# Kernel optimization log

Hardware: AMD Instinct MI355X
Metric: run time of the kernel (lower is better)

## Reference

```python
import jax, jax.numpy as jnp
import numpy as np
from jax import lax

H, W = 4096, 4096

def setup_inputs() -> dict:
    key = jax.random.key(0)
    k_occ, k_seed = jax.random.split(key)
    occupied = (jax.random.uniform(k_occ, (H, W)) < 0.3).astype(jnp.float32)
    flood = ((jax.random.uniform(k_seed, (H, W)) < 1e-3).astype(jnp.float32)
             * (1.0 - occupied))
    flood_input = jnp.stack([occupied, flood], axis=-1)  # [H, W, 2]
    flood_count = jnp.zeros((H, W), dtype=jnp.float32)
    # Fixed flood kernel, HWIO layout: (3, 3, in=2, out=1)
    kernel = jnp.zeros((3, 3, 2, 1), dtype=jnp.float32)
    kernel = kernel.at[1, 1, 0, 0].set(-5.0)  # occupied center blocks flood
    kernel = kernel.at[1, 2, 1, 0].set(1.0)   # right
    kernel = kernel.at[2, 1, 1, 0].set(1.0)   # down
    kernel = kernel.at[1, 0, 1, 0].set(1.0)   # left
    kernel = kernel.at[0, 1, 1, 0].set(1.0)   # up
    kernel = kernel.at[1, 1, 1, 0].set(1.0)   # center
    bias = jnp.zeros((1,), dtype=jnp.float32)
    return {"flood_input": flood_input, "flood_count": flood_count,
            "kernel": kernel, "bias": bias, "num_steps": 16}

def reference(flood_input, flood_count, kernel, bias, num_steps):
    dn = ("NHWC", "HWIO", "NHWC")

    def flood_step(carry, _):
        x, count = carry                      # x: [H, W, 2], count: [H, W]
        occupied = x[..., 0]
        y = lax.conv_general_dilated(x[None], kernel, (1, 1), "SAME",
                                     dimension_numbers=dn)[0, ..., 0] + bias[0]
        y = jnp.clip(y, 0.0, 1.0)             # flooded frontier
        new_x = jnp.stack([occupied, y], axis=-1)
        return (new_x, count + y), None

    (x_final, count_final), _ = lax.scan(flood_step,
                                         (flood_input, flood_count),
                                         None, length=num_steps)
    # [H, W, 3]: occupied, flood, count
    return jnp.concatenate([x_final, count_final[..., None]], axis=-1)
```

## Files before the change

### kernel.cpp

```cpp
#include <hip/hip_runtime.h>


typedef unsigned long long u64;
typedef float f32x4 __attribute__((ext_vector_type(4)));
typedef float f32x2 __attribute__((ext_vector_type(2)));

#define HH 4096
#define WW 4096
#define WPR 64
#define NSTEPS 16
#define HALO 16
#define IT 32

__global__ __launch_bounds__(256) void pack_kernel(
    const float* __restrict__ flood_input,
    u64* __restrict__ occP, u64* __restrict__ flP)
{
    const int lane = threadIdx.x & 63;
    const int wv   = threadIdx.x >> 6;
    const int r    = blockIdx.x;
#pragma unroll
    for (int b = 0; b < 2; ++b) {
        float vx[8], vy[8];
#pragma unroll
        for (int j = 0; j < 8; ++j) {
            const int w = wv * 16 + b * 8 + j;
            const f32x2 v = __builtin_nontemporal_load(
                (const f32x2*)(flood_input +
                                ((size_t)r * WW + (w << 6) + lane) * 2));
            vx[j] = v[0]; vy[j] = v[1];
        }
#pragma unroll
        for (int j = 0; j < 8; ++j) {
            const int w = wv * 16 + b * 8 + j;
            const u64 om = __ballot(vx[j] > 0.5f);
            const u64 fm = __ballot(vy[j] > 0.5f);
            if (lane == 0) {
                occP[(size_t)r * WPR + w] = om;
                flP [(size_t)r * WPR + w] = fm;
            }
        }
    }
}

__global__ __launch_bounds__(256, 8) void flood_kernel(
    const u64* __restrict__ occP, const u64* __restrict__ flP,
    const float* __restrict__ flood_count,
    float* __restrict__ out)
{
    __shared__ u64 plane[4][IT][7];
    __shared__ float out2[4][2 * 128 * 3];

    const int tid  = threadIdx.x;
    const int lane = tid & 63;
    const int wv   = tid >> 6;

    const int wgid = blockIdx.y * 32 + blockIdx.x;
    const int nl   = (wgid & 7) * 512 + (wgid >> 3);
    const int bx   = nl & 31;
    const int by   = nl >> 5;

    const int tile_r0 = by * IT;
    const int tile_c0 = bx * (4 * IT) + wv * IT;
    const int bc0     = bx * (4 * IT);

    const int gr  = tile_r0 - HALO + lane;
    const bool rin = (gr >= 0) & (gr < HH);
    const int s   = tile_c0 - HALO;
    const int q0  = ((s + 64) >> 6) - 1;
    const int sh  = s - (q0 << 6);

    const size_t base = (size_t)(rin ? gr : 0) * WPR;
    const int qa = min(max(q0, 0), WPR - 1);
    const int qb = min(max(q0 + 1, 0), WPR - 1);
    u64 o0 = occP[base + qa], o1 = occP[base + qb];
    u64 f0 = flP [base + qa], f1 = flP [base + qb];
    const bool va = rin & (q0 >= 0);
    const bool vb = rin & (q0 + 1 < WPR);
    if (!va) { o0 = ~0ull; f0 = 0ull; }
    if (!vb) { o1 = ~0ull; f1 = 0ull; }
    const u64 occ = (o0 >> sh) | (sh ? (o1 << (64 - sh)) : 0ull);
    u64       f   = (f0 >> sh) | (sh ? (f1 << (64 - sh)) : 0ull);

    const int half = lane >> 5;
    const int l32  = lane & 31;
    const int col0 = l32 * 4;
    const float* fcbase = flood_count +
        (size_t)(tile_r0 + wv * 8 + half) * WW + bc0 + col0;
    f32x4 fc_next = __builtin_nontemporal_load((const f32x4*)fcbase);

    const u64 nocc = ~occ;
    u64 c0 = 0, c1 = 0, c2 = 0, c3 = 0, c4 = 0;
#pragma unroll
    for (int it = 0; it < NSTEPS; ++it) {
        u64 up = __shfl_up(f, 1);
        u64 dn = __shfl_down(f, 1);
        if (lane == 0)  up = 0ull;
        if (lane == 63) dn = 0ull;
        f = nocc & (f | (f << 1) | (f >> 1) | up | dn);
        u64 c = f, t;
        t = c0; c0 = t ^ c; c = t & c;
        t = c1; c1 = t ^ c; c = t & c;
        t = c2; c2 = t ^ c; c = t & c;
        t = c3; c3 = t ^ c; c = t & c;
        c4 ^= c;
    }

    if (lane >= HALO && lane < HALO + IT) {
        u64* p = plane[wv][lane - HALO];
        p[0] = occ; p[1] = f;
        p[2] = c0; p[3] = c1; p[4] = c2; p[5] = c3; p[6] = c4;
    }
    __syncthreads();

    const int sw   = col0 >> 5;
    const int bit0 = HALO + (col0 & 31);
    for (int t = 0; t < 4; ++t) {
        const f32x4 fc4 = fc_next;
        if (t + 1 < 4)
            fc_next = __builtin_nontemporal_load(
                (const f32x4*)(fcbase + (size_t)(t + 1) * 2 * WW));

        const int rA   = wv * 8 + 2 * t;
        const int irow = rA + half;
        const u64* p = plane[sw][irow];
        const u64 ow = p[0], fw = p[1];
        const u64 k0 = p[2], k1 = p[3], k2 = p[4], k3 = p[5], k4 = p[6];

        float v[12];
#pragma unroll
        for (int j = 0; j < 4; ++j) {
            const int bit = bit0 + j;
            int cv = (int)((k0 >> bit) & 1ull)
                   + ((int)((k1 >> bit) & 1ull) << 1)
                   + ((int)((k2 >> bit) & 1ull) << 2)
                   + ((int)((k3 >> bit) & 1ull) << 3)
                   + ((int)((k4 >> bit) & 1ull) << 4);
            v[j*3+0] = (float)((ow >> bit) & 1ull);
            v[j*3+1] = (float)((fw >> bit) & 1ull);
            v[j*3+2] = (float)cv + fc4[j];
        }
        float* dst = &out2[wv][half * 384 + l32 * 12];
        *(f32x4*)(dst + 0) = (f32x4){v[0], v[1], v[2],  v[3]};
        *(f32x4*)(dst + 4) = (f32x4){v[4], v[5], v[6],  v[7]};
        *(f32x4*)(dst + 8) = (f32x4){v[8], v[9], v[10], v[11]};

        __syncthreads();

#pragma unroll
        for (int st = 0; st < 3; ++st) {
            const int L   = st * 256 + lane * 4;
            const int row = (L >= 384) ? 1 : 0;
            const int off = L - row * 384;
            const f32x4 q = *(const f32x4*)(&out2[wv][L]);
            *(f32x4*)(out + ((size_t)(tile_r0 + rA + row) * WW + bc0) * 3
                      + off) = q;
        }
    }
}

extern "C" void kernel_launch(void* const* d_in, const int* in_sizes, int n_in,
                              void* d_out, int out_size, void* d_ws, size_t ws_size,
                              hipStream_t stream) {
    const float* flood_input = (const float*)d_in[0];
    const float* flood_cnt   = (const float*)d_in[1];
    float* out = (float*)d_out;

    u64* occP = (u64*)d_ws;
    u64* flP  = occP + (size_t)HH * WPR;

    pack_kernel<<<dim3(HH), dim3(256), 0, stream>>>(flood_input, occP, flP);

    dim3 grid(WW / (4 * IT), HH / IT);
    flood_kernel<<<grid, dim3(256), 0, stream>>>(occP, flP, flood_cnt, out);
}
```

Before: 358.7 us.

## Fuse bit-packing of the input grid into the flood kernel

Removes the separate pack kernel and its bitmask buffers in the workspace. Each wave now loads its own 64x64 halo window of float2 input straight from global memory and builds the occupancy and flood bitmasks in registers with wave ballots. This drops one kernel launch and the write-then-read of the intermediate bitmasks. In exchange, overlapping halo windows are re-read about four times per input element, and a serial 16-iteration load-and-ballot loop now sits in front of the compute.

```diff
diff --git a/kernel.cpp b/kernel.cpp
--- a/kernel.cpp
+++ b/kernel.cpp
@@ -7,44 +7,12 @@
 
 #define HH 4096
 #define WW 4096
-#define WPR 64
 #define NSTEPS 16
 #define HALO 16
 #define IT 32
 
-__global__ __launch_bounds__(256) void pack_kernel(
+__global__ __launch_bounds__(256, 8) void flood_kernel(
     const float* __restrict__ flood_input,
-    u64* __restrict__ occP, u64* __restrict__ flP)
-{
-    const int lane = threadIdx.x & 63;
-    const int wv   = threadIdx.x >> 6;
-    const int r    = blockIdx.x;
-#pragma unroll
-    for (int b = 0; b < 2; ++b) {
-        float vx[8], vy[8];
-#pragma unroll
-        for (int j = 0; j < 8; ++j) {
-            const int w = wv * 16 + b * 8 + j;
-            const f32x2 v = __builtin_nontemporal_load(
-                (const f32x2*)(flood_input +
-                                ((size_t)r * WW + (w << 6) + lane) * 2));
-            vx[j] = v[0]; vy[j] = v[1];
-        }
-#pragma unroll
-        for (int j = 0; j < 8; ++j) {
-            const int w = wv * 16 + b * 8 + j;
-            const u64 om = __ballot(vx[j] > 0.5f);
-            const u64 fm = __ballot(vy[j] > 0.5f);
-            if (lane == 0) {
-                occP[(size_t)r * WPR + w] = om;
-                flP [(size_t)r * WPR + w] = fm;
-            }
-        }
-    }
-}
-
-__global__ __launch_bounds__(256, 8) void flood_kernel(
-    const u64* __restrict__ occP, const u64* __restrict__ flP,
     const float* __restrict__ flood_count,
     float* __restrict__ out)
 {
@@ -64,30 +32,43 @@
     const int tile_c0 = bx * (4 * IT) + wv * IT;
     const int bc0     = bx * (4 * IT);
 
-    const int gr  = tile_r0 - HALO + lane;
-    const bool rin = (gr >= 0) & (gr < HH);
-    const int s   = tile_c0 - HALO;
-    const int q0  = ((s + 64) >> 6) - 1;
-    const int sh  = s - (q0 << 6);
-
-    const size_t base = (size_t)(rin ? gr : 0) * WPR;
-    const int qa = min(max(q0, 0), WPR - 1);
-    const int qb = min(max(q0 + 1, 0), WPR - 1);
-    u64 o0 = occP[base + qa], o1 = occP[base + qb];
-    u64 f0 = flP [base + qa], f1 = flP [base + qb];
-    const bool va = rin & (q0 >= 0);
-    const bool vb = rin & (q0 + 1 < WPR);
-    if (!va) { o0 = ~0ull; f0 = 0ull; }
-    if (!vb) { o1 = ~0ull; f1 = 0ull; }
-    const u64 occ = (o0 >> sh) | (sh ? (o1 << (64 - sh)) : 0ull);
-    u64       f   = (f0 >> sh) | (sh ? (f1 << (64 - sh)) : 0ull);
-
     const int half = lane >> 5;
     const int l32  = lane & 31;
     const int col0 = l32 * 4;
     const float* fcbase = flood_count +
         (size_t)(tile_r0 + wv * 8 + half) * WW + bc0 + col0;
     f32x4 fc_next = __builtin_nontemporal_load((const f32x4*)fcbase);
+
+    const int gc   = tile_c0 - HALO + lane;
+    const bool cin = (gc >= 0) & (gc < WW);
+    const int gcc  = min(max(gc, 0), WW - 1);
+    const u64 colmask = __ballot(cin);
+    const int r0 = tile_r0 - HALO;
+    const float* ibase = flood_input + (size_t)gcc * 2;
+
+    u64 occ = 0, f = 0;
+#pragma unroll 1
+    for (int jb = 0; jb < 64; jb += 4) {
+        f32x2 v[4];
+#pragma unroll
+        for (int j = 0; j < 4; ++j) {
+            const int gr  = r0 + jb + j;
+            const int grc = min(max(gr, 0), HH - 1);
+            v[j] = *(const f32x2*)(ibase + (size_t)grc * (WW * 2));
+        }
+#pragma unroll
+        for (int j = 0; j < 4; ++j) {
+            const int gr = r0 + jb + j;
+            u64 om = __ballot(v[j][0] > 0.5f);
+            u64 fm = __ballot(v[j][1] > 0.5f);
+            om |= ~colmask;
+            fm &= colmask;
+            if (gr < 0 || gr >= HH) { om = ~0ull; fm = 0ull; }
+            const bool mine = (lane == jb + j);
+            occ = mine ? om : occ;
+            f   = mine ? fm : f;
+        }
+    }
 
     const u64 nocc = ~occ;
     u64 c0 = 0, c1 = 0, c2 = 0, c3 = 0, c4 = 0;
@@ -166,11 +147,6 @@
     const float* flood_cnt   = (const float*)d_in[1];
     float* out = (float*)d_out;
 
-    u64* occP = (u64*)d_ws;
-    u64* flP  = occP + (size_t)HH * WPR;
-
-    pack_kernel<<<dim3(HH), dim3(256), 0, stream>>>(flood_input, occP, flP);
-
     dim3 grid(WW / (4 * IT), HH / IT);
-    flood_kernel<<<grid, dim3(256), 0, stream>>>(occP, flP, flood_cnt, out);
+    flood_kernel<<<grid, dim3(256), 0, stream>>>(flood_input, flood_cnt, out);
 }
```

Measured after the change: 363.4 us. Within noise of the previous version (+1.3%).
